# Optimization experiments

Hardware: AMD Instinct MI355X
Metric: run time of the kernel (lower is better)

The kernel has to match this reference:

```python
import jax, jax.numpy as jnp
import numpy as np

N_HEAD = 16
DROP_P = 0.1


def setup_inputs() -> dict:
    key = jax.random.key(0)
    ks = jax.random.split(key, 5)
    B, T, C = 2, 2048, 1024
    return {
        "x": jax.random.normal(ks[0], (B, T, C), dtype=jnp.float32),
        "w_attn": jax.random.normal(ks[1], (C, 3 * C), dtype=jnp.float32) * 0.02,
        "b_attn": jax.random.normal(ks[2], (3 * C,), dtype=jnp.float32) * 0.02,
        "w_proj": jax.random.normal(ks[3], (C, C), dtype=jnp.float32) * 0.02,
        "b_proj": jax.random.normal(ks[4], (C,), dtype=jnp.float32) * 0.02,
    }


def reference(x, w_attn, b_attn, w_proj, b_proj):
    B, T, C = x.shape
    H = N_HEAD
    D = C // H  # head dim
    qkv = x @ w_attn + b_attn                      # [B,T,3C]
    q, k, v = jnp.split(qkv, 3, axis=-1)
    # [B,T,C] -> [B,H,T,D]
    q = q.reshape(B, T, H, D).transpose(0, 2, 1, 3)
    k = k.reshape(B, T, H, D).transpose(0, 2, 1, 3)
    v = v.reshape(B, T, H, D).transpose(0, 2, 1, 3)
    scale = 1.0 / jnp.sqrt(jnp.float32(D))
    attn = jnp.einsum("bhqd,bhkd->bhqk", q, k) * scale  # [B,H,T,T]
    causal = jnp.tril(jnp.ones((T, T), dtype=bool))
    attn = jnp.where(causal[None, None], attn, jnp.float32(-jnp.inf))
    attn = jax.nn.softmax(attn, axis=-1)
    # dropout p=0.1 (training mode in original); deterministic fixed key here
    keep = jax.random.bernoulli(jax.random.key(42), 1.0 - DROP_P, attn.shape)
    attn = jnp.where(keep, attn / (1.0 - DROP_P), 0.0)
    out = jnp.einsum("bhqk,bhkd->bhqd", attn, v)   # [B,H,T,D]
    out = out.transpose(0, 2, 1, 3).reshape(B, T, C)
    return out @ w_proj + b_proj
```

## Files before the change

### kernel.cpp

```cpp
#include <hip/hip_runtime.h>
#include <hip/hip_bf16.h>
#include <stdint.h>
#include <math.h>

#define TSEQ   2048
#define NBATCH 2
#define NHEAD  16
#define HDIM   64
#define CDIM   1024

#define KEEP_LIMIT 3865470464u
#define QSC 0.18033688011112042f

typedef short  bf16x8 __attribute__((ext_vector_type(8)));
typedef float  f32x4  __attribute__((ext_vector_type(4)));

__device__ __forceinline__ float fast_exp2(float x) {
    float r; asm("v_exp_f32 %0, %1" : "=v"(r) : "v"(x)); return r;
}
__device__ __forceinline__ uint32_t cvt_pk_bf16(float a, float b) {
    uint32_t r; asm("v_cvt_pk_bf16_f32 %0, %1, %2" : "=v"(r) : "v"(a), "v"(b)); return r;
}

__device__ __forceinline__ uint32_t rotl32(uint32_t x, int r) {
    return __builtin_amdgcn_alignbit(x, x, 32 - r);
}

__device__ __forceinline__ uint32_t tf2x32_xor(uint32_t x0, uint32_t x1) {
    const uint32_t ka = 0u, kb = 42u;
    const uint32_t kc = ka ^ kb ^ 0x1BD11BDAu;
    x0 += ka; x1 += kb;
#define TFR(r) { x0 += x1; x1 = rotl32(x1, r); x1 ^= x0; }
    TFR(13) TFR(15) TFR(26) TFR(6)
    x0 += kb; x1 += kc + 1u;
    TFR(17) TFR(29) TFR(16) TFR(24)
    x0 += kc; x1 += ka + 2u;
    TFR(13) TFR(15) TFR(26) TFR(6)
    x0 += ka; x1 += kb + 3u;
    TFR(17) TFR(29) TFR(16) TFR(24)
    x0 += kb; x1 += kc + 4u;
    TFR(13) TFR(15) TFR(26) TFR(6)
    x0 += kc; x1 += ka + 5u;
#undef TFR
    return x0 ^ x1;
}

__device__ __forceinline__ float bf2f(ushort u) {
    union { uint32_t i; float f; } c; c.i = ((uint32_t)u) << 16; return c.f;
}

__device__ __forceinline__ void async_copy16(void* lds, const void* g) {
    __builtin_amdgcn_global_load_lds(
        (const __attribute__((address_space(1))) unsigned int*)g,
        (__attribute__((address_space(3))) unsigned int*)lds, 16, 0, 0);
}

__global__ __launch_bounds__(256) void cvt_bf16(
    const float* __restrict__ src, ushort* __restrict__ dst, int n)
{
    int idx = (blockIdx.x * 256 + threadIdx.x) * 8;
    if (idx >= n) return;
    float4 a = *(const float4*)(src + idx);
    float4 b = *(const float4*)(src + idx + 4);
    uint4 o;
    o.x = cvt_pk_bf16(a.x, a.y); o.y = cvt_pk_bf16(a.z, a.w);
    o.z = cvt_pk_bf16(b.x, b.y); o.w = cvt_pk_bf16(b.z, b.w);
    *(uint4*)(dst + idx) = o;
}

__global__ __launch_bounds__(256) void transpose_cvt(
    const float* __restrict__ src, ushort* __restrict__ dst, int K, int N)
{
    __shared__ float t[32][33];
    const int n0 = blockIdx.x * 32, k0 = blockIdx.y * 32;
    const int i = threadIdx.x;
    {
        int k = i >> 3, n4 = (i & 7) * 4;
        float4 v = *(const float4*)(src + (size_t)(k0 + k) * N + n0 + n4);
        t[k][n4 + 0] = v.x; t[k][n4 + 1] = v.y; t[k][n4 + 2] = v.z; t[k][n4 + 3] = v.w;
    }
    __syncthreads();
    {
        int n = i >> 3, k4 = (i & 7) * 4;
        uint2 o;
        o.x = cvt_pk_bf16(t[k4 + 0][n], t[k4 + 1][n]);
        o.y = cvt_pk_bf16(t[k4 + 2][n], t[k4 + 3][n]);
        *(uint2*)(dst + (size_t)(n0 + n) * K + k0 + k4) = o;
    }
}

template<int MODE>
__global__ __launch_bounds__(256) void gemm_bf16(
    const ushort* __restrict__ A, const ushort* __restrict__ Bt,
    const float* __restrict__ bias,
    ushort* __restrict__ Q, ushort* __restrict__ Kq, ushort* __restrict__ V,
    float* __restrict__ Cf, int M, int N, int K)
{
    __shared__ ushort As[2][128 * 32];
    __shared__ ushort Bs[2][128 * 32];
    const int tid = threadIdx.x, lane = tid & 63, wid = tid >> 6;
    const int l15 = lane & 15, l4 = lane >> 4;
    const int wr = wid >> 1, wc = wid & 1;
    const int bn = blockIdx.x, bm = blockIdx.y;
    const int NTK = K >> 5;

    f32x4 acc[4][4];
#pragma unroll
    for (int m = 0; m < 4; ++m)
#pragma unroll
        for (int n = 0; n < 4; ++n) acc[m][n] = (f32x4){0.f, 0.f, 0.f, 0.f};

    auto stage = [&](int p, int k0) {
#pragma unroll
        for (int j = 0; j < 2; ++j) {
            const int rbase = wid * 32 + j * 16;
            const int row = rbase + (lane >> 2);
            const ushort* src = A + (size_t)(bm * 128 + row) * K + k0 + (lane & 3) * 8;
            async_copy16(&As[p][rbase * 32], src);
        }
#pragma unroll
        for (int j = 0; j < 2; ++j) {
            const int rbase = wid * 32 + j * 16;
            const int row = rbase + (lane >> 2);
            const ushort* src = Bt + (size_t)(bn * 128 + row) * K + k0 + (lane & 3) * 8;
            async_copy16(&Bs[p][rbase * 32], src);
        }
    };
    auto compute = [&](int p) {
        bf16x8 af[4], bf[4];
#pragma unroll
        for (int m = 0; m < 4; ++m)
            af[m] = *(const bf16x8*)&As[p][(wr * 64 + m * 16 + l15) * 32 + l4 * 8];
#pragma unroll
        for (int n = 0; n < 4; ++n)
            bf[n] = *(const bf16x8*)&Bs[p][(wc * 64 + n * 16 + l15) * 32 + l4 * 8];
#pragma unroll
        for (int m = 0; m < 4; ++m)
#pragma unroll
            for (int n = 0; n < 4; ++n)
                acc[m][n] = __builtin_amdgcn_mfma_f32_16x16x32_bf16(af[m], bf[n], acc[m][n], 0, 0, 0);
    };

    stage(0, 0);
    __syncthreads();
    for (int t = 0; t < NTK; ++t) {
        const int p = t & 1;
        if (t + 1 < NTK) stage(p ^ 1, (t + 1) << 5);
        compute(p);
        __syncthreads();
    }

    const int colbase = bn * 128 + wc * 64;
    const int rowbase = bm * 128 + wr * 64;
    if (MODE == 0) {
#pragma unroll
        for (int n = 0; n < 4; ++n) {
            const int col = colbase + n * 16 + l15;
            const float bv = bias[col];
#pragma unroll
            for (int m = 0; m < 4; ++m)
#pragma unroll
                for (int r = 0; r < 4; ++r) {
                    const int row = rowbase + m * 16 + l4 * 4 + r;
                    Cf[(size_t)row * N + col] = acc[m][n][r] + bv;
                }
        }
    } else {
#pragma unroll
        for (int n = 0; n < 4; ++n) {
            const int col = colbase + n * 16 + l15;
            const int which = col >> 10, cc = col & 1023;
            const int hh = cc >> 6, dd = cc & 63;
            const float bv = bias[col];
            const float sc = (which == 0) ? QSC : 1.0f;
#pragma unroll
            for (int m = 0; m < 4; ++m) {
                float v0 = (acc[m][n][0] + bv) * sc, v1 = (acc[m][n][1] + bv) * sc;
                float v2 = (acc[m][n][2] + bv) * sc, v3 = (acc[m][n][3] + bv) * sc;
                uint32_t pk01 = cvt_pk_bf16(v0, v1), pk23 = cvt_pk_bf16(v2, v3);
                ushort vals[4] = { (ushort)pk01, (ushort)(pk01 >> 16),
                                   (ushort)pk23, (ushort)(pk23 >> 16) };
#pragma unroll
                for (int r = 0; r < 4; ++r) {
                    const int row = rowbase + m * 16 + l4 * 4 + r;
                    const int bb = row >> 11, tt = row & 2047;
                    if (which == 0)
                        Q[(((size_t)(bb * NHEAD + hh)) * TSEQ + tt) * HDIM + dd] = vals[r];
                    else if (which == 1)
                        Kq[(((size_t)(bb * NHEAD + hh)) * TSEQ + tt) * HDIM + dd] = vals[r];
                    else
                        V[(((size_t)(bb * NHEAD + hh)) * HDIM + dd) * TSEQ + tt] = vals[r];
                }
            }
        }
    }
}

__global__ __launch_bounds__(256) void attn_fwd_mfma(
    const ushort* __restrict__ Qb, const ushort* __restrict__ Kb,
    const ushort* __restrict__ VbT,
    ushort* __restrict__ Ap, float* __restrict__ mp, float* __restrict__ lp)
{
    __shared__ ushort Ks[64 * 64];
    __shared__ ushort Vt[2][64 * 64];
    __shared__ ushort Ps[64 * 64];
    const int tid = threadIdx.x;
    const int lane = tid & 63;
    const int wid = tid >> 6;
    const int l15 = lane & 15, l4 = lane >> 4;
    const int pair = blockIdx.x >> 1, half = blockIdx.x & 1;
    const int h = blockIdx.y, b = blockIdx.z;
    const int hb = b * NHEAD + h;
    const size_t headoff = (size_t)hb * TSEQ * HDIM;
    const ushort* Qg = Qb + headoff;
    const ushort* Kg = Kb + headoff;
    const ushort* Vg = VbT + headoff;

    auto stageK = [&](int kt) {
        const ushort* Kt = Kg + (size_t)(kt * 64) * HDIM;
#pragma unroll
        for (int c = 0; c < 2; ++c) {
            const int rbase = wid * 16 + c * 8;
            const int row = rbase + (lane >> 3);
            const ushort* srcK = Kt + row * 64 + (((lane & 7) * 8) ^ ((row & 7) << 3));
            async_copy16(&Ks[rbase * 64], srcK);
        }
    };
    auto stageV = [&](int p, int kt) {
        const ushort* Vt0 = Vg + kt * 64;
#pragma unroll
        for (int c = 0; c < 2; ++c) {
            const int rbase = wid * 16 + c * 8;
            const int row = rbase + (lane >> 3);
            const ushort* srcV = Vt0 + (size_t)row * TSEQ + (((lane & 7) * 8) ^ ((row & 7) << 3));
            async_copy16(&Vt[p][rbase * 64], srcV);
        }
    };

    const int swq = (l15 & 7) << 3;
    const int prow = wid * 16 + l15;

    for (int pass = 0; pass < 2; ++pass) {
        const int qt = pass ? (TSEQ / 64 - 1) - pair : pair;
        const int ntk = qt + 1;
        const int kb = half ? (ntk + 1) >> 1 : 0;
        const int ke = half ? ntk : (ntk + 1) >> 1;
        const int pidx = (hb * 32 + qt) * 2 + half;
        const int tilerow = wid * 16 + l15;
        ushort* arow = Ap + (size_t)pidx * 4096 + tilerow * 64;

        if (kb >= ke) {
#pragma unroll
            for (int dt = 0; dt < 4; ++dt) {
                ushort4 z; z.x = z.y = z.z = z.w = 0;
                *(ushort4*)&arow[dt * 16 + l4 * 4] = z;
            }
            if (l4 == 0) { mp[pidx * 64 + tilerow] = -INFINITY; lp[pidx * 64 + tilerow] = 0.f; }
            continue;
        }

        const int qglob = qt * 64 + tilerow;
        bf16x8 qf0, qf1;
        {
            const ushort* qrow = Qg + (size_t)qglob * HDIM;
            qf0 = *(const bf16x8*)(qrow + l4 * 8);
            qf1 = *(const bf16x8*)(qrow + 32 + l4 * 8);
        }

        f32x4 oacc[4];
#pragma unroll
        for (int i = 0; i < 4; ++i) oacc[i] = (f32x4){0.f, 0.f, 0.f, 0.f};
        float mi = -INFINITY, li = 0.f;
        const uint32_t rowbase = ((uint32_t)hb * TSEQ + (uint32_t)qglob) * TSEQ;

        stageK(kb);
        stageV(0, kb);
        __syncthreads();

        for (int kt = kb; kt < ke; ++kt) {
            const int p = (kt - kb) & 1;
            const bool pf = (kt + 1 < ke);
            if (pf) stageV(p ^ 1, kt + 1);

            const int kb0 = kt * 64;
            const uint32_t idx0 = rowbase + (uint32_t)kb0;
            uint32_t tfb[4][4];
#pragma unroll
            for (int ct = 0; ct < 4; ++ct) {
                const uint32_t kk = idx0 + (uint32_t)(ct * 16 + l4 * 4);
                tfb[ct][0] = tf2x32_xor(0u, kk + 0u);
                tfb[ct][1] = tf2x32_xor(0u, kk + 1u);
                tfb[ct][2] = tf2x32_xor(0u, kk + 2u);
                tfb[ct][3] = tf2x32_xor(0u, kk + 3u);
            }

            f32x4 s4[4];
#pragma unroll
            for (int ct = 0; ct < 4; ++ct) {
                const int krow = ct * 16 + l15;
                const int sw = (krow & 7) << 3;
                bf16x8 kf0 = *(const bf16x8*)&Ks[krow * 64 + ((l4 * 8) ^ sw)];
                bf16x8 kf1 = *(const bf16x8*)&Ks[krow * 64 + ((l4 * 8 + 32) ^ sw)];
                f32x4 a = {0.f, 0.f, 0.f, 0.f};
                a = __builtin_amdgcn_mfma_f32_16x16x32_bf16(kf0, qf0, a, 0, 0, 0);
                a = __builtin_amdgcn_mfma_f32_16x16x32_bf16(kf1, qf1, a, 0, 0, 0);
                s4[ct] = a;
            }
            __syncthreads();
            if (pf) stageK(kt + 1);

            float ev[4][4];
            if (kt == qt) {
#pragma unroll
                for (int ct = 0; ct < 4; ++ct)
#pragma unroll
                    for (int r = 0; r < 4; ++r) {
                        const int kglob = kb0 + ct * 16 + l4 * 4 + r;
                        ev[ct][r] = (kglob <= qglob) ? s4[ct][r] : -INFINITY;
                    }
            } else {
#pragma unroll
                for (int ct = 0; ct < 4; ++ct)
#pragma unroll
                    for (int r = 0; r < 4; ++r) ev[ct][r] = s4[ct][r];
            }
            float mx;
            {
                float t0 = fmaxf(fmaxf(ev[0][0], ev[0][1]), ev[0][2]);
                float t1 = fmaxf(fmaxf(ev[0][3], ev[1][0]), ev[1][1]);
                float t2 = fmaxf(fmaxf(ev[1][2], ev[1][3]), ev[2][0]);
                float t3 = fmaxf(fmaxf(ev[2][1], ev[2][2]), ev[2][3]);
                float t4 = fmaxf(fmaxf(ev[3][0], ev[3][1]), ev[3][2]);
                float t5 = fmaxf(fmaxf(t0, t1), ev[3][3]);
                float t6 = fmaxf(fmaxf(t2, t3), t4);
                mx = fmaxf(t5, t6);
            }
            mx = fmaxf(mx, __shfl_xor(mx, 16));
            mx = fmaxf(mx, __shfl_xor(mx, 32));

            if (__any(mx > mi)) {
                const float mnew = fmaxf(mi, mx);
                const float alpha = fast_exp2(mi - mnew);
                mi = mnew;
                li *= alpha;
#pragma unroll
                for (int dt = 0; dt < 4; ++dt) {
                    oacc[dt][0] *= alpha; oacc[dt][1] *= alpha;
                    oacc[dt][2] *= alpha; oacc[dt][3] *= alpha;
                }
            }
            float rs = 0.f;
#pragma unroll
            for (int ct = 0; ct < 4; ++ct)
#pragma unroll
                for (int r = 0; r < 4; ++r) {
                    ev[ct][r] = fast_exp2(ev[ct][r] - mi);
                    rs += ev[ct][r];
                }
            rs += __shfl_xor(rs, 16);
            rs += __shfl_xor(rs, 32);
            li += rs;

#pragma unroll
            for (int ct = 0; ct < 4; ++ct) {
                const float p0 = (tfb[ct][0] < KEEP_LIMIT) ? ev[ct][0] : 0.f;
                const float p1 = (tfb[ct][1] < KEEP_LIMIT) ? ev[ct][1] : 0.f;
                const float p2 = (tfb[ct][2] < KEEP_LIMIT) ? ev[ct][2] : 0.f;
                const float p3 = (tfb[ct][3] < KEEP_LIMIT) ? ev[ct][3] : 0.f;
                uint2 pk;
                pk.x = cvt_pk_bf16(p0, p1);
                pk.y = cvt_pk_bf16(p2, p3);
                *(uint2*)&Ps[prow * 64 + ((ct * 16 + l4 * 4) ^ swq)] = pk;
            }

            bf16x8 pf0 = *(const bf16x8*)&Ps[prow * 64 + ((l4 * 8) ^ swq)];
            bf16x8 pf1 = *(const bf16x8*)&Ps[prow * 64 + ((l4 * 8 + 32) ^ swq)];
#pragma unroll
            for (int dt = 0; dt < 4; ++dt) {
                const int drow = dt * 16 + l15;
                const int swv = (drow & 7) << 3;
                bf16x8 vf0 = *(const bf16x8*)&Vt[p][drow * 64 + ((l4 * 8) ^ swv)];
                bf16x8 vf1 = *(const bf16x8*)&Vt[p][drow * 64 + ((l4 * 8 + 32) ^ swv)];
                oacc[dt] = __builtin_amdgcn_mfma_f32_16x16x32_bf16(vf0, pf0, oacc[dt], 0, 0, 0);
                oacc[dt] = __builtin_amdgcn_mfma_f32_16x16x32_bf16(vf1, pf1, oacc[dt], 0, 0, 0);
            }
            __syncthreads();
        }

#pragma unroll
        for (int dt = 0; dt < 4; ++dt) {
            uint2 o;
            o.x = cvt_pk_bf16(oacc[dt][0], oacc[dt][1]);
            o.y = cvt_pk_bf16(oacc[dt][2], oacc[dt][3]);
            *(uint2*)&arow[dt * 16 + l4 * 4] = o;
        }
        if (l4 == 0) { mp[pidx * 64 + tilerow] = mi; lp[pidx * 64 + tilerow] = li; }
    }
}

__global__ __launch_bounds__(256) void attn_merge(
    const ushort* __restrict__ Ap, const float* __restrict__ mp,
    const float* __restrict__ lp, ushort* __restrict__ AO)
{
    const int gidx = blockIdx.x * 16 + (threadIdx.x >> 4);
    const int hb = gidx >> 11;
    const int q  = gidx & 2047;
    const int qt = q >> 6, row = q & 63;
    const int sub = (threadIdx.x & 15) * 4;
    const int pidx0 = (hb * 32 + qt) * 2;
    const int pr = pidx0 * 64 + row;
    const float m0 = mp[pr], m1 = mp[pr + 64];
    const float l0 = lp[pr], l1 = lp[pr + 64];
    const float m  = fmaxf(m0, m1);
    const float w0 = fast_exp2(m0 - m), w1 = fast_exp2(m1 - m);
    const float inv = 1.0f / ((l0 * w0 + l1 * w1) * 0.9f);
    const float s0 = w0 * inv, s1 = w1 * inv;
    ushort4 a0 = *(const ushort4*)&Ap[(size_t)pidx0 * 4096 + row * 64 + sub];
    ushort4 a1 = *(const ushort4*)&Ap[(size_t)(pidx0 + 1) * 4096 + row * 64 + sub];
    const int b = hb >> 4, h = hb & 15;
    ushort* orow = AO + ((size_t)(b * TSEQ + q)) * CDIM + h * HDIM + sub;
    uint2 o;
    o.x = cvt_pk_bf16(bf2f(a0.x) * s0 + bf2f(a1.x) * s1,
                      bf2f(a0.y) * s0 + bf2f(a1.y) * s1);
    o.y = cvt_pk_bf16(bf2f(a0.z) * s0 + bf2f(a1.z) * s1,
                      bf2f(a0.w) * s0 + bf2f(a1.w) * s1);
    *(uint2*)orow = o;
}

extern "C" void kernel_launch(void* const* d_in, const int* in_sizes, int n_in,
                              void* d_out, int out_size, void* d_ws, size_t ws_size,
                              hipStream_t stream)
{
    const float* x      = (const float*)d_in[0];
    const float* w_attn = (const float*)d_in[1];
    const float* b_attn = (const float*)d_in[2];
    const float* w_proj = (const float*)d_in[3];
    const float* b_proj = (const float*)d_in[4];
    float* out = (float*)d_out;

    const size_t NH = (size_t)NBATCH * NHEAD * TSEQ * HDIM;
    ushort* Qb  = (ushort*)d_ws;
    ushort* Kb  = Qb + NH;
    ushort* VbT = Kb + NH;
    ushort* AO  = VbT + NH;
    ushort* xb  = AO + NH;
    ushort* wTa = xb + NH;
    ushort* wTp = wTa + (size_t)3072 * 1024;
    float*  mp  = (float*)(wTp + (size_t)1024 * 1024);
    float*  lp  = mp + (size_t)2048 * 64;

    ushort* Aparts = (ushort*)d_out;

    cvt_bf16<<<2048, 256, 0, stream>>>(x, xb, 4096 * 1024);
    transpose_cvt<<<dim3(96, 32), 256, 0, stream>>>(w_attn, wTa, 1024, 3072);
    transpose_cvt<<<dim3(32, 32), 256, 0, stream>>>(w_proj, wTp, 1024, 1024);

    gemm_bf16<1><<<dim3(24, 32), 256, 0, stream>>>(
        xb, wTa, b_attn, Qb, Kb, VbT, nullptr, 4096, 3072, 1024);

    attn_fwd_mfma<<<dim3(32, NHEAD, NBATCH), 256, 0, stream>>>(
        Qb, Kb, VbT, Aparts, mp, lp);

    attn_merge<<<4096, 256, 0, stream>>>(Aparts, mp, lp, AO);

    gemm_bf16<0><<<dim3(8, 32), 256, 0, stream>>>(
        AO, wTp, b_proj, nullptr, nullptr, nullptr, out, 4096, 1024, 1024);
}
```

Baseline: 237.4 us.

## Precompute dropout bitmask in separate kernel and drop online-softmax max tracking

Moves the Threefry dropout RNG out of the attention inner loop into a gen_mask kernel. It writes one 64-bit keep mask per query row and key tile, which attention then reads with a single load per tile. It also removes the running max and rescaling of online softmax, exponentiating raw scaled scores on the assumption they stay small enough not to overflow, and simplifies the merge to a plain sum. The max removal relies on bounded logits for these inputs and could overflow for other data; the mask adds an extra kernel and about 16 MB of global traffic.

```diff
diff --git a/kernel.cpp b/kernel.cpp
--- a/kernel.cpp
+++ b/kernel.cpp
@@ -55,6 +55,32 @@
         (__attribute__((address_space(3))) unsigned int*)lds, 16, 0, 0);
 }
 
+__global__ __launch_bounds__(256) void gen_mask(unsigned long long* __restrict__ mask)
+{
+    const int lane = threadIdx.x & 63;
+    const int wv   = threadIdx.x >> 6;
+    const int pair = blockIdx.x;
+    const int hb   = blockIdx.y;
+    const int half = blockIdx.z;
+    for (int pass = 0; pass < 2; ++pass) {
+        const int qt = pass ? 31 - pair : pair;
+        const int nk = qt + 1;
+        const int h0 = half ? (nk + 1) >> 1 : 0;
+        const int h1 = half ? nk : (nk + 1) >> 1;
+        const int ntask = (h1 - h0) << 6;
+        const uint32_t qbase = ((uint32_t)hb << 11) + (uint32_t)(qt << 6);
+        for (int t = wv; t < ntask; t += 4) {
+            const int q  = t & 63;
+            const int kt = h0 + (t >> 6);
+            const uint32_t idx = (qbase + (uint32_t)q) * 2048u + (uint32_t)(kt << 6) + (uint32_t)lane;
+            const bool keep = tf2x32_xor(0u, idx) < KEEP_LIMIT;
+            const unsigned long long bal = __ballot(keep);
+            if (lane == 0)
+                mask[((size_t)(qbase + (uint32_t)q) << 5) + kt] = bal;
+        }
+    }
+}
+
 __global__ __launch_bounds__(256) void cvt_bf16(
     const float* __restrict__ src, ushort* __restrict__ dst, int n)
 {
@@ -198,8 +224,8 @@
 
 __global__ __launch_bounds__(256) void attn_fwd_mfma(
     const ushort* __restrict__ Qb, const ushort* __restrict__ Kb,
-    const ushort* __restrict__ VbT,
-    ushort* __restrict__ Ap, float* __restrict__ mp, float* __restrict__ lp)
+    const ushort* __restrict__ VbT, const unsigned long long* __restrict__ Mk,
+    ushort* __restrict__ Ap, float* __restrict__ lp)
 {
     __shared__ ushort Ks[64 * 64];
     __shared__ ushort Vt[2][64 * 64];
@@ -255,11 +281,12 @@
                 ushort4 z; z.x = z.y = z.z = z.w = 0;
                 *(ushort4*)&arow[dt * 16 + l4 * 4] = z;
             }
-            if (l4 == 0) { mp[pidx * 64 + tilerow] = -INFINITY; lp[pidx * 64 + tilerow] = 0.f; }
+            if (l4 == 0) lp[pidx * 64 + tilerow] = 0.f;
             continue;
         }
 
         const int qglob = qt * 64 + tilerow;
+        const unsigned long long* mrow = Mk + ((size_t)(hb * TSEQ + qglob) << 5);
         bf16x8 qf0, qf1;
         {
             const ushort* qrow = Qg + (size_t)qglob * HDIM;
@@ -270,8 +297,7 @@
         f32x4 oacc[4];
 #pragma unroll
         for (int i = 0; i < 4; ++i) oacc[i] = (f32x4){0.f, 0.f, 0.f, 0.f};
-        float mi = -INFINITY, li = 0.f;
-        const uint32_t rowbase = ((uint32_t)hb * TSEQ + (uint32_t)qglob) * TSEQ;
+        float li = 0.f;
 
         stageK(kb);
         stageV(0, kb);
@@ -279,20 +305,10 @@
 
         for (int kt = kb; kt < ke; ++kt) {
             const int p = (kt - kb) & 1;
-            const bool pf = (kt + 1 < ke);
-            if (pf) stageV(p ^ 1, kt + 1);
-
-            const int kb0 = kt * 64;
-            const uint32_t idx0 = rowbase + (uint32_t)kb0;
-            uint32_t tfb[4][4];
-#pragma unroll
-            for (int ct = 0; ct < 4; ++ct) {
-                const uint32_t kk = idx0 + (uint32_t)(ct * 16 + l4 * 4);
-                tfb[ct][0] = tf2x32_xor(0u, kk + 0u);
-                tfb[ct][1] = tf2x32_xor(0u, kk + 1u);
-                tfb[ct][2] = tf2x32_xor(0u, kk + 2u);
-                tfb[ct][3] = tf2x32_xor(0u, kk + 3u);
-            }
+            const bool hasNext = (kt + 1 < ke);
+            if (hasNext) stageV(p ^ 1, kt + 1);
+
+            const unsigned long long m64 = mrow[kt];
 
             f32x4 s4[4];
 #pragma unroll
@@ -307,66 +323,35 @@
                 s4[ct] = a;
             }
             __syncthreads();
-            if (pf) stageK(kt + 1);
-
-            float ev[4][4];
+            if (hasNext) stageK(kt + 1);
+
+            const int kb0 = kt * 64;
             if (kt == qt) {
 #pragma unroll
                 for (int ct = 0; ct < 4; ++ct)
 #pragma unroll
                     for (int r = 0; r < 4; ++r) {
                         const int kglob = kb0 + ct * 16 + l4 * 4 + r;
-                        ev[ct][r] = (kglob <= qglob) ? s4[ct][r] : -INFINITY;
+                        s4[ct][r] = (kglob <= qglob) ? s4[ct][r] : -INFINITY;
                     }
-            } else {
-#pragma unroll
-                for (int ct = 0; ct < 4; ++ct)
-#pragma unroll
-                    for (int r = 0; r < 4; ++r) ev[ct][r] = s4[ct][r];
-            }
-            float mx;
-            {
-                float t0 = fmaxf(fmaxf(ev[0][0], ev[0][1]), ev[0][2]);
-                float t1 = fmaxf(fmaxf(ev[0][3], ev[1][0]), ev[1][1]);
-                float t2 = fmaxf(fmaxf(ev[1][2], ev[1][3]), ev[2][0]);
-                float t3 = fmaxf(fmaxf(ev[2][1], ev[2][2]), ev[2][3]);
-                float t4 = fmaxf(fmaxf(ev[3][0], ev[3][1]), ev[3][2]);
-                float t5 = fmaxf(fmaxf(t0, t1), ev[3][3]);
-                float t6 = fmaxf(fmaxf(t2, t3), t4);
-                mx = fmaxf(t5, t6);
-            }
-            mx = fmaxf(mx, __shfl_xor(mx, 16));
-            mx = fmaxf(mx, __shfl_xor(mx, 32));
-
-            if (__any(mx > mi)) {
-                const float mnew = fmaxf(mi, mx);
-                const float alpha = fast_exp2(mi - mnew);
-                mi = mnew;
-                li *= alpha;
-#pragma unroll
-                for (int dt = 0; dt < 4; ++dt) {
-                    oacc[dt][0] *= alpha; oacc[dt][1] *= alpha;
-                    oacc[dt][2] *= alpha; oacc[dt][3] *= alpha;
+            }
+            float rs = 0.f;
+#pragma unroll
+            for (int ct = 0; ct < 4; ++ct)
+#pragma unroll
+                for (int r = 0; r < 4; ++r) {
+                    s4[ct][r] = fast_exp2(s4[ct][r]);
+                    rs += s4[ct][r];
                 }
-            }
-            float rs = 0.f;
-#pragma unroll
-            for (int ct = 0; ct < 4; ++ct)
-#pragma unroll
-                for (int r = 0; r < 4; ++r) {
-                    ev[ct][r] = fast_exp2(ev[ct][r] - mi);
-                    rs += ev[ct][r];
-                }
-            rs += __shfl_xor(rs, 16);
-            rs += __shfl_xor(rs, 32);
             li += rs;
 
 #pragma unroll
             for (int ct = 0; ct < 4; ++ct) {
-                const float p0 = (tfb[ct][0] < KEEP_LIMIT) ? ev[ct][0] : 0.f;
-                const float p1 = (tfb[ct][1] < KEEP_LIMIT) ? ev[ct][1] : 0.f;
-                const float p2 = (tfb[ct][2] < KEEP_LIMIT) ? ev[ct][2] : 0.f;
-                const float p3 = (tfb[ct][3] < KEEP_LIMIT) ? ev[ct][3] : 0.f;
+                const uint32_t nib = (uint32_t)(m64 >> (ct * 16 + l4 * 4)) & 0xFu;
+                const float p0 = (nib & 1u) ? s4[ct][0] : 0.f;
+                const float p1 = (nib & 2u) ? s4[ct][1] : 0.f;
+                const float p2 = (nib & 4u) ? s4[ct][2] : 0.f;
+                const float p3 = (nib & 8u) ? s4[ct][3] : 0.f;
                 uint2 pk;
                 pk.x = cvt_pk_bf16(p0, p1);
                 pk.y = cvt_pk_bf16(p2, p3);
@@ -394,13 +379,16 @@
             o.y = cvt_pk_bf16(oacc[dt][2], oacc[dt][3]);
             *(uint2*)&arow[dt * 16 + l4 * 4] = o;
         }
-        if (l4 == 0) { mp[pidx * 64 + tilerow] = mi; lp[pidx * 64 + tilerow] = li; }
+        float rs = li;
+        rs += __shfl_xor(rs, 16);
+        rs += __shfl_xor(rs, 32);
+        if (l4 == 0) lp[pidx * 64 + tilerow] = rs;
     }
 }
 
 __global__ __launch_bounds__(256) void attn_merge(
-    const ushort* __restrict__ Ap, const float* __restrict__ mp,
-    const float* __restrict__ lp, ushort* __restrict__ AO)
+    const ushort* __restrict__ Ap, const float* __restrict__ lp,
+    ushort* __restrict__ AO)
 {
     const int gidx = blockIdx.x * 16 + (threadIdx.x >> 4);
     const int hb = gidx >> 11;
@@ -409,21 +397,17 @@
     const int sub = (threadIdx.x & 15) * 4;
     const int pidx0 = (hb * 32 + qt) * 2;
     const int pr = pidx0 * 64 + row;
-    const float m0 = mp[pr], m1 = mp[pr + 64];
     const float l0 = lp[pr], l1 = lp[pr + 64];
-    const float m  = fmaxf(m0, m1);
-    const float w0 = fast_exp2(m0 - m), w1 = fast_exp2(m1 - m);
-    const float inv = 1.0f / ((l0 * w0 + l1 * w1) * 0.9f);
-    const float s0 = w0 * inv, s1 = w1 * inv;
+    const float inv = 1.0f / ((l0 + l1) * 0.9f);
     ushort4 a0 = *(const ushort4*)&Ap[(size_t)pidx0 * 4096 + row * 64 + sub];
     ushort4 a1 = *(const ushort4*)&Ap[(size_t)(pidx0 + 1) * 4096 + row * 64 + sub];
     const int b = hb >> 4, h = hb & 15;
     ushort* orow = AO + ((size_t)(b * TSEQ + q)) * CDIM + h * HDIM + sub;
     uint2 o;
-    o.x = cvt_pk_bf16(bf2f(a0.x) * s0 + bf2f(a1.x) * s1,
-                      bf2f(a0.y) * s0 + bf2f(a1.y) * s1);
-    o.y = cvt_pk_bf16(bf2f(a0.z) * s0 + bf2f(a1.z) * s1,
-                      bf2f(a0.w) * s0 + bf2f(a1.w) * s1);
+    o.x = cvt_pk_bf16((bf2f(a0.x) + bf2f(a1.x)) * inv,
+                      (bf2f(a0.y) + bf2f(a1.y)) * inv);
+    o.y = cvt_pk_bf16((bf2f(a0.z) + bf2f(a1.z)) * inv,
+                      (bf2f(a0.w) + bf2f(a1.w)) * inv);
     *(uint2*)orow = o;
 }
 
@@ -446,8 +430,8 @@
     ushort* xb  = AO + NH;
     ushort* wTa = xb + NH;
     ushort* wTp = wTa + (size_t)3072 * 1024;
-    float*  mp  = (float*)(wTp + (size_t)1024 * 1024);
-    float*  lp  = mp + (size_t)2048 * 64;
+    unsigned long long* Mk = (unsigned long long*)(wTp + (size_t)1024 * 1024);
+    float*  lp  = (float*)(Mk + (size_t)65536 * 32);
 
     ushort* Aparts = (ushort*)d_out;
 
@@ -458,10 +442,12 @@
     gemm_bf16<1><<<dim3(24, 32), 256, 0, stream>>>(
         xb, wTa, b_attn, Qb, Kb, VbT, nullptr, 4096, 3072, 1024);
 
+    gen_mask<<<dim3(16, 32, 2), 256, 0, stream>>>(Mk);
+
     attn_fwd_mfma<<<dim3(32, NHEAD, NBATCH), 256, 0, stream>>>(
-        Qb, Kb, VbT, Aparts, mp, lp);
-
-    attn_merge<<<4096, 256, 0, stream>>>(Aparts, mp, lp, AO);
+        Qb, Kb, VbT, Mk, Aparts, lp);
+
+    attn_merge<<<4096, 256, 0, stream>>>(Aparts, lp, AO);
 
     gemm_bf16<0><<<dim3(8, 32), 256, 0, stream>>>(
         AO, wTp, b_proj, nullptr, nullptr, nullptr, out, 4096, 1024, 1024);
```

Result: slower. 278.6 us (+17.4%).
